# Kernel tuning notes

Hardware: AMD Instinct MI355X
Metric: run time of the kernel (lower is better)

## Reference

```python
import jax, jax.numpy as jnp
import numpy as np

N, E, Q = 50000, 500000, 100000
IN_DIM, HID, EDGE_DIM, NUM_CLASSES = 128, 128, 16, 2


def _glorot(key, shape):
    fan_in, fan_out = shape
    lim = (6.0 / (fan_in + fan_out)) ** 0.5
    return jax.random.uniform(key, shape, jnp.float32, -lim, lim)


def setup_inputs() -> dict:
    key = jax.random.key(0)
    ks = jax.random.split(key, 12)
    return {
        "node_feature": jax.random.normal(ks[0], (N, IN_DIM), jnp.float32),
        "edge_index": jax.random.randint(ks[1], (2, E), 0, N, jnp.int64),
        "edge_feature": jax.random.normal(ks[2], (E, EDGE_DIM), jnp.float32),
        "edge_label_index": jax.random.randint(ks[3], (2, Q), 0, N, jnp.int64),
        # conv1 params
        "c1_pre_W": _glorot(ks[4], (IN_DIM, IN_DIM)),
        "c1_pre_b": jnp.zeros((IN_DIM,), jnp.float32),
        "c1_msg_W": _glorot(ks[5], (2 * IN_DIM + EDGE_DIM, HID)),
        "c1_msg_b": jnp.zeros((HID,), jnp.float32),
        # conv2 params
        "c2_pre_W": _glorot(ks[6], (HID, HID)),
        "c2_pre_b": jnp.zeros((HID,), jnp.float32),
        "c2_msg_W": _glorot(ks[7], (2 * HID + EDGE_DIM, HID)),
        "c2_msg_b": jnp.zeros((HID,), jnp.float32),
        # link-prediction head
        "lp_W": _glorot(ks[8], (2 * HID, NUM_CLASSES)),
        "lp_b": jnp.zeros((NUM_CLASSES,), jnp.float32),
    }


def _mlp_message_conv(x, edge_index, edge_feature, pre_W, pre_b, msg_W, msg_b):
    # pre_conv: Linear + ReLU
    h = jax.nn.relu(x @ pre_W + pre_b)
    src, dst = edge_index[0], edge_index[1]
    # PyG default flow source_to_target: x_i = target, x_j = source
    x_i = h[dst]  # [E, d]
    x_j = h[src]  # [E, d]
    msg = jnp.concatenate([x_i, x_j, edge_feature], axis=1) @ msg_W + msg_b  # [E, out]
    # aggr='add' onto target nodes
    return jax.ops.segment_sum(msg, dst, num_segments=x.shape[0])


def reference(node_feature, edge_index, edge_feature, edge_label_index,
              c1_pre_W, c1_pre_b, c1_msg_W, c1_msg_b,
              c2_pre_W, c2_pre_b, c2_msg_W, c2_msg_b,
              lp_W, lp_b):
    # eval mode: dropout is identity
    x = jax.nn.relu(_mlp_message_conv(node_feature, edge_index, edge_feature,
                                      c1_pre_W, c1_pre_b, c1_msg_W, c1_msg_b))
    x = _mlp_message_conv(x, edge_index, edge_feature,
                          c2_pre_W, c2_pre_b, c2_msg_W, c2_msg_b)
    nodes_first = x[edge_label_index[0]]   # [Q, hid]
    nodes_second = x[edge_label_index[1]]  # [Q, hid]
    pred = jnp.concatenate([nodes_first, nodes_second], axis=-1) @ lp_W + lp_b
    return pred
```

## Files before the change

kernel.cpp:

```cpp
#include <hip/hip_runtime.h>
#include <cstdint>
#include <cstddef>


typedef __attribute__((ext_vector_type(8))) short short8;
typedef __attribute__((ext_vector_type(4))) float float4v;

__device__ __forceinline__ ushort f2b(float f) {
    uint u = __float_as_uint(f);
    u = u + 0x7fff + ((u >> 16) & 1);
    return (ushort)(u >> 16);
}
__device__ __forceinline__ float b2f(ushort h) {
    return __uint_as_float(((uint)h) << 16);
}
__device__ __forceinline__ uint pack2(float a, float b) {
    return (uint)f2b(a) | ((uint)f2b(b) << 16);
}

#define F_MSG     1
#define F_RELU    2
#define F_DEGBIAS 4
#define F_OUTB    8
#define F_IN32    16
#define F_HEAD    32

#define XS_STRIDE 72

__launch_bounds__(256, 2)
__global__ void gemm_mfma(const ushort* __restrict__ A, const ushort* __restrict__ B,
                          const ushort* __restrict__ EF, const float* __restrict__ A32,
                          const float* __restrict__ DEG, const ushort* __restrict__ Wt,
                          const float* __restrict__ bias, ushort* __restrict__ outB,
                          const float* __restrict__ lpW, float* __restrict__ z,
                          int M, int Kp, int flags)
{
    __shared__ ushort xs[128 * XS_STRIDE];
    __shared__ ushort ws[128 * XS_STRIDE];
    const int tid  = threadIdx.x;
    const int lane = tid & 63;
    const int wave = tid >> 6;
    const int row0 = blockIdx.x << 7;

    float4v acc[2][8];
#pragma unroll
    for (int m = 0; m < 2; ++m)
#pragma unroll
        for (int t = 0; t < 8; ++t) acc[m][t] = (float4v){0.f, 0.f, 0.f, 0.f};

    const int arow0 = (wave << 5) + (lane & 15);
    const int koff  = (lane >> 4) << 3;
    const int bcol  = lane & 15;

    for (int kt = 0; kt < Kp; kt += 64) {
        __syncthreads();
        for (int idx = tid; idx < 128 * 8; idx += 256) {
            const int n = idx >> 3;
            const int g = idx & 7;
            const uint4 v = *(const uint4*)&Wt[(size_t)n * Kp + kt + (g << 3)];
            *(uint4*)&ws[n * XS_STRIDE + (g << 3)] = v;
        }
        if (flags & F_MSG) {
            for (int idx = tid; idx < 128 * 8; idx += 256) {
                const int r  = idx >> 3;
                const int g  = idx & 7;
                const int gr = row0 + r;
                const int kk = kt + (g << 3);
                uint4 v = make_uint4(0, 0, 0, 0);
                if (gr < M) {
                    if (kk < 128) {
                        uint4 a = *(const uint4*)&A[((size_t)gr << 7) + kk];
                        const float d = DEG[gr];
                        uint* p = (uint*)&a;
#pragma unroll
                        for (int q = 0; q < 4; ++q)
                            p[q] = pack2(b2f((ushort)(p[q] & 0xffff)) * d,
                                         b2f((ushort)(p[q] >> 16)) * d);
                        v = a;
                    } else if (kk < 256) {
                        v = *(const uint4*)&B[((size_t)gr << 7) + kk - 128];
                    } else if (kk < 272) {
                        v = *(const uint4*)&EF[((size_t)gr << 4) + kk - 256];
                    }
                }
                *(uint4*)&xs[r * XS_STRIDE + (g << 3)] = v;
            }
        } else if (flags & F_IN32) {
            for (int idx = tid; idx < 128 * 8; idx += 256) {
                const int r  = idx >> 3;
                const int g  = idx & 7;
                const int gr = row0 + r;
                uint4 v = make_uint4(0, 0, 0, 0);
                if (gr < M) {
                    const float4 f0 = *(const float4*)&A32[((size_t)gr << 7) + kt + (g << 3)];
                    const float4 f1 = *(const float4*)&A32[((size_t)gr << 7) + kt + (g << 3) + 4];
                    v.x = pack2(f0.x, f0.y); v.y = pack2(f0.z, f0.w);
                    v.z = pack2(f1.x, f1.y); v.w = pack2(f1.z, f1.w);
                }
                *(uint4*)&xs[r * XS_STRIDE + (g << 3)] = v;
            }
        } else {
            for (int idx = tid; idx < 128 * 8; idx += 256) {
                const int r  = idx >> 3;
                const int g  = idx & 7;
                const int gr = row0 + r;
                uint4 v = make_uint4(0, 0, 0, 0);
                if (gr < M) v = *(const uint4*)&A[((size_t)gr << 7) + kt + (g << 3)];
                *(uint4*)&xs[r * XS_STRIDE + (g << 3)] = v;
            }
        }
        __syncthreads();
#pragma unroll
        for (int s = 0; s < 64; s += 32) {
            const short8 a0 = *(const short8*)&xs[arow0 * XS_STRIDE + s + koff];
            const short8 a1 = *(const short8*)&xs[(arow0 + 16) * XS_STRIDE + s + koff];
#pragma unroll
            for (int t = 0; t < 8; ++t) {
                const short8 bf = *(const short8*)&ws[((t << 4) + bcol) * XS_STRIDE + s + koff];
                acc[0][t] = __builtin_amdgcn_mfma_f32_16x16x32_bf16(a0, bf, acc[0][t], 0, 0, 0);
                acc[1][t] = __builtin_amdgcn_mfma_f32_16x16x32_bf16(a1, bf, acc[1][t], 0, 0, 0);
            }
        }
    }

    float bcv[8];
#pragma unroll
    for (int t = 0; t < 8; ++t) bcv[t] = bias[(t << 4) + bcol];

    if (flags & F_HEAD) {
        const float2* lw = (const float2*)lpW;
        float2 wa[8], wb[8];
#pragma unroll
        for (int t = 0; t < 8; ++t) {
            const int col = (t << 4) + bcol;
            wa[t] = lw[col];
            wb[t] = lw[128 + col];
        }
#pragma unroll
        for (int m = 0; m < 2; ++m) {
            const int rbase = row0 + (wave << 5) + (m << 4) + ((lane >> 4) << 2);
#pragma unroll
            for (int r = 0; r < 4; ++r) {
                const int row = rbase + r;
                const float d = (row < M) ? DEG[row] : 0.f;
                float za0 = 0.f, za1 = 0.f, zb0 = 0.f, zb1 = 0.f;
#pragma unroll
                for (int t = 0; t < 8; ++t) {
                    const float v = acc[m][t][r] + d * bcv[t];
                    za0 += v * wa[t].x; za1 += v * wa[t].y;
                    zb0 += v * wb[t].x; zb1 += v * wb[t].y;
                }
#pragma unroll
                for (int mk = 8; mk > 0; mk >>= 1) {
                    za0 += __shfl_xor(za0, mk);
                    za1 += __shfl_xor(za1, mk);
                    zb0 += __shfl_xor(zb0, mk);
                    zb1 += __shfl_xor(zb1, mk);
                }
                if (bcol == 0 && row < M)
                    *(float4*)&z[(size_t)row * 4] = make_float4(za0, za1, zb0, zb1);
            }
        }
    } else {
#pragma unroll
        for (int m = 0; m < 2; ++m) {
            const int rbase = row0 + (wave << 5) + (m << 4) + ((lane >> 4) << 2);
#pragma unroll
            for (int t = 0; t < 8; ++t) {
                const int col = (t << 4) + bcol;
#pragma unroll
                for (int r = 0; r < 4; ++r) {
                    const int row = rbase + r;
                    if (row >= M) continue;
                    float v = acc[m][t][r];
                    v += (flags & F_DEGBIAS) ? DEG[row] * bcv[t] : bcv[t];
                    if (flags & F_RELU) v = fmaxf(v, 0.f);
                    outB[((size_t)row << 7) + col] = f2b(v);
                }
            }
        }
    }
}

__launch_bounds__(256)
__global__ void prep(const float* __restrict__ c1pW, const float* __restrict__ c2pW,
                     const float* __restrict__ c1mW, const float* __restrict__ c2mW,
                     ushort* __restrict__ wtp1, ushort* __restrict__ wtp2,
                     ushort* __restrict__ wtm1, ushort* __restrict__ wtm2,
                     int* __restrict__ counts, int N)
{
    const int gtid = blockIdx.x * 256 + threadIdx.x;
    const int gstr = gridDim.x * 256;
    for (int i = gtid; i < N; i += gstr) counts[i] = 0;
    for (int idx = gtid; idx < 128 * 128; idx += gstr) {
        const int n = idx >> 7, k = idx & 127;
        wtp1[idx] = f2b(c1pW[(size_t)k * 128 + n]);
        wtp2[idx] = f2b(c2pW[(size_t)k * 128 + n]);
    }
    for (int idx = gtid; idx < 128 * 320; idx += gstr) {
        const int n = idx / 320, k = idx - n * 320;
        wtm1[idx] = (k < 272) ? f2b(c1mW[(size_t)k * 128 + n]) : (ushort)0;
        wtm2[idx] = (k < 272) ? f2b(c2mW[(size_t)k * 128 + n]) : (ushort)0;
    }
}

__launch_bounds__(256)
__global__ void hist_kernel(const int* __restrict__ ei, int* __restrict__ counts, int E)
{
    const int e = blockIdx.x * 256 + threadIdx.x;
    if (e < E) atomicAdd(&counts[ei[E + e]], 1);
}

__launch_bounds__(256)
__global__ void scan_phase1(const int* __restrict__ counts, int* __restrict__ rowstart,
                            int* __restrict__ blocksums, int N)
{
    __shared__ int sdata[256];
    const int t = threadIdx.x;
    const int i = blockIdx.x * 256 + t;
    const int v = (i < N) ? counts[i] : 0;
    sdata[t] = v;
    __syncthreads();
    for (int off = 1; off < 256; off <<= 1) {
        const int add = (t >= off) ? sdata[t - off] : 0;
        __syncthreads();
        sdata[t] += add;
        __syncthreads();
    }
    if (i < N) rowstart[i] = sdata[t] - v;
    if (t == 255) blocksums[blockIdx.x] = sdata[255];
}

__launch_bounds__(256)
__global__ void scan_phase23(const int* __restrict__ counts, const int* __restrict__ bs,
                             int* __restrict__ rowstart, int* __restrict__ cursor,
                             float* __restrict__ degf, int N, int E)
{
    __shared__ int sdata[256];
    const int t = threadIdx.x;
    const int vb = blockIdx.x;
    int part = 0;
    for (int j = t; j < vb; j += 256) part += bs[j];
    sdata[t] = part;
    __syncthreads();
    for (int s = 128; s > 0; s >>= 1) {
        if (t < s) sdata[t] += sdata[t + s];
        __syncthreads();
    }
    const int off = sdata[0];
    const int i = vb * 256 + t;
    if (i < N) {
        const int rs = rowstart[i] + off;
        rowstart[i] = rs;
        cursor[i]   = rs;
        degf[i]     = (float)counts[i];
    }
    if (vb == 0 && t == 0) rowstart[N] = E;
}

__launch_bounds__(256)
__global__ void build_elist(const int* __restrict__ ei, int* __restrict__ cursor,
                            int* __restrict__ esrc, int* __restrict__ eeid, int E)
{
    const int e = blockIdx.x * 256 + threadIdx.x;
    if (e >= E) return;
    const int d = ei[E + e];
    const int pos = atomicAdd(&cursor[d], 1);
    esrc[pos] = ei[e];
    eeid[pos] = e;
}

__launch_bounds__(256)
__global__ void gather(const int* __restrict__ esrc, const int* __restrict__ eeid,
                       const int* __restrict__ rowstart,
                       const ushort* __restrict__ h, ushort* __restrict__ agg,
                       const float* __restrict__ ef, ushort* __restrict__ aggef,
                       int N, int doEf)
{
    const int tid = threadIdx.x;
    if (doEf) {
        const int nvb = (N + 15) / 16;
        const int lane16 = tid & 15;
        for (int vb = blockIdx.x; vb < nvb; vb += gridDim.x) {
            const int node = vb * 16 + (tid >> 4);
            if (node >= N) continue;
            const int beg = rowstart[node];
            const int end = rowstart[node + 1];
            float acc = 0.f;
            for (int k = beg; k < end; ++k)
                acc += ef[((size_t)eeid[k] << 4) + lane16];
            aggef[((size_t)node << 4) + lane16] = f2b(acc);
        }
    }
    {
        const int nvb = (N + 3) / 4;
        const int lane = tid & 63;
        const int wave = tid >> 6;
        for (int vb = blockIdx.x; vb < nvb; vb += gridDim.x) {
            const int node = vb * 4 + wave;
            if (node >= N) continue;
            const int beg = rowstart[node];
            const int end = rowstart[node + 1];
            float ax = 0.f, ay = 0.f;
            int k = beg;
            for (; k + 3 < end; k += 4) {
                const int s0 = esrc[k];
                const int s1 = esrc[k + 1];
                const int s2 = esrc[k + 2];
                const int s3 = esrc[k + 3];
                const uint v0 = *(const uint*)&h[((size_t)s0 << 7) + (lane << 1)];
                const uint v1 = *(const uint*)&h[((size_t)s1 << 7) + (lane << 1)];
                const uint v2 = *(const uint*)&h[((size_t)s2 << 7) + (lane << 1)];
                const uint v3 = *(const uint*)&h[((size_t)s3 << 7) + (lane << 1)];
                ax += b2f((ushort)(v0 & 0xffff)) + b2f((ushort)(v1 & 0xffff))
                    + b2f((ushort)(v2 & 0xffff)) + b2f((ushort)(v3 & 0xffff));
                ay += b2f((ushort)(v0 >> 16)) + b2f((ushort)(v1 >> 16))
                    + b2f((ushort)(v2 >> 16)) + b2f((ushort)(v3 >> 16));
            }
            for (; k < end; ++k) {
                const uint v = *(const uint*)&h[((size_t)esrc[k] << 7) + (lane << 1)];
                ax += b2f((ushort)(v & 0xffff));
                ay += b2f((ushort)(v >> 16));
            }
            *(uint*)&agg[((size_t)node << 7) + (lane << 1)] = pack2(ax, ay);
        }
    }
}

__launch_bounds__(256)
__global__ void head_kernel(const float4* __restrict__ z, const int* __restrict__ eli,
                            const float* __restrict__ lpb, float* __restrict__ out, int Q)
{
    const int q = blockIdx.x * 256 + threadIdx.x;
    if (q >= Q) return;
    const int a = eli[q];
    const int b = eli[Q + q];
    const float4 za = z[a];
    const float4 zb = z[b];
    float2 o = make_float2(za.x + zb.z + lpb[0], za.y + zb.w + lpb[1]);
    *(float2*)&out[(size_t)q * 2] = o;
}

extern "C" void kernel_launch(void* const* d_in, const int* in_sizes, int n_in,
                              void* d_out, int out_size, void* d_ws, size_t ws_size,
                              hipStream_t stream)
{
    const float* nf   = (const float*)d_in[0];
    const int*   ei   = (const int*)d_in[1];
    const float* ef   = (const float*)d_in[2];
    const int*   eli  = (const int*)d_in[3];
    const float* c1pW = (const float*)d_in[4];
    const float* c1pb = (const float*)d_in[5];
    const float* c1mW = (const float*)d_in[6];
    const float* c1mb = (const float*)d_in[7];
    const float* c2pW = (const float*)d_in[8];
    const float* c2pb = (const float*)d_in[9];
    const float* c2mW = (const float*)d_in[10];
    const float* c2mb = (const float*)d_in[11];
    const float* lpW  = (const float*)d_in[12];
    const float* lpb  = (const float*)d_in[13];
    float* out = (float*)d_out;

    const int N = in_sizes[0] / 128;
    const int E = in_sizes[1] / 2;
    const int Q = in_sizes[3] / 2;

    float* DEG = (float*)d_ws;
    float* z   = DEG + N;
    int* counts    = (int*)(z + (size_t)N * 4);
    int* rowstart  = counts + N;
    int* cursor    = rowstart + N + 1;
    int* blocksums = cursor + N;
    int* esrc      = blocksums + 1024;
    int* eeid      = esrc + E;
    uintptr_t up = (uintptr_t)(eeid + E);
    up = (up + 15) & ~(uintptr_t)15;
    ushort* h_bf   = (ushort*)up;
    ushort* agg_bf = h_bf   + (size_t)N * 128;
    ushort* x1_bf  = agg_bf + (size_t)N * 128;
    ushort* ef_bf  = x1_bf  + (size_t)N * 128;
    ushort* wtp1   = ef_bf  + (size_t)N * 16;
    ushort* wtm1   = wtp1 + 128 * 128;
    ushort* wtp2   = wtm1 + 128 * 320;
    ushort* wtm2   = wtp2 + 128 * 128;

    const int gemmGrid = (N + 127) / 128;
    const int eGrid    = (E + 255) / 256;
    const int nGrid    = (N + 255) / 256;
    const int gGrid    = (N + 3) / 4;
    const int headGrid = (Q + 255) / 256;

    prep<<<nGrid, 256, 0, stream>>>(c1pW, c2pW, c1mW, c2mW, wtp1, wtp2, wtm1, wtm2,
                                    counts, N);
    hist_kernel<<<eGrid, 256, 0, stream>>>(ei, counts, E);
    scan_phase1<<<nGrid, 256, 0, stream>>>(counts, rowstart, blocksums, N);
    scan_phase23<<<nGrid, 256, 0, stream>>>(counts, blocksums, rowstart, cursor, DEG, N, E);
    build_elist<<<eGrid, 256, 0, stream>>>(ei, cursor, esrc, eeid, E);

    gemm_mfma<<<gemmGrid, 256, 0, stream>>>(nullptr, nullptr, nullptr, nf, DEG, wtp1,
                                            c1pb, h_bf, nullptr, nullptr, N, 128,
                                            F_RELU | F_OUTB | F_IN32);
    gather<<<gGrid, 256, 0, stream>>>(esrc, eeid, rowstart, h_bf, agg_bf, ef, ef_bf, N, 1);
    gemm_mfma<<<gemmGrid, 256, 0, stream>>>(h_bf, agg_bf, ef_bf, nullptr, DEG, wtm1,
                                            c1mb, x1_bf, nullptr, nullptr, N, 320,
                                            F_MSG | F_RELU | F_DEGBIAS | F_OUTB);

    gemm_mfma<<<gemmGrid, 256, 0, stream>>>(x1_bf, nullptr, nullptr, nullptr, DEG, wtp2,
                                            c2pb, h_bf, nullptr, nullptr, N, 128,
                                            F_RELU | F_OUTB);
    gather<<<gGrid, 256, 0, stream>>>(esrc, eeid, rowstart, h_bf, agg_bf, nullptr, nullptr, N, 0);
    gemm_mfma<<<gemmGrid, 256, 0, stream>>>(h_bf, agg_bf, ef_bf, nullptr, DEG, wtm2,
                                            c2mb, nullptr, lpW, z, N, 320,
                                            F_MSG | F_DEGBIAS | F_HEAD);

    head_kernel<<<headGrid, 256, 0, stream>>>((const float4*)z, eli, lpb, out, Q);
}
```

Measured before the change: 331.8 us.

## Split node features into column halves and pin each half to an XCD group

The pre-conv GEMMs now write h in a planar layout of two 64-column halves. The gather kernel maps blocks so that XCDs 0-3 only read the first half and XCDs 4-7 only the second, using 32 lanes per node. The message GEMM's A load is adjusted to read the split layout. The goal is to shrink each XCD's random-gather working set so more of it stays in its L2, at the cost of relying on round-robin block-to-XCD dispatch and issuing narrower 128-byte row reads.

```diff
diff --git a/kernel.cpp b/kernel.cpp
--- a/kernel.cpp
+++ b/kernel.cpp
@@ -24,6 +24,7 @@
 #define F_OUTB    8
 #define F_IN32    16
 #define F_HEAD    32
+#define F_OUTH    64
 
 #define XS_STRIDE 72
 
@@ -51,6 +52,7 @@
     const int arow0 = (wave << 5) + (lane & 15);
     const int koff  = (lane >> 4) << 3;
     const int bcol  = lane & 15;
+    const size_t halfSz = (size_t)M * 64;
 
     for (int kt = 0; kt < Kp; kt += 64) {
         __syncthreads();
@@ -69,7 +71,9 @@
                 uint4 v = make_uint4(0, 0, 0, 0);
                 if (gr < M) {
                     if (kk < 128) {
-                        uint4 a = *(const uint4*)&A[((size_t)gr << 7) + kk];
+                        const int hh = kk >> 6;
+                        uint4 a = *(const uint4*)&A[(size_t)hh * halfSz
+                                                    + ((size_t)gr << 6) + (kk & 63)];
                         const float d = DEG[gr];
                         uint* p = (uint*)&a;
 #pragma unroll
@@ -168,6 +172,10 @@
 #pragma unroll
             for (int t = 0; t < 8; ++t) {
                 const int col = (t << 4) + bcol;
+                const size_t obase = (flags & F_OUTH)
+                    ? (size_t)(col >> 6) * halfSz + (col & 63)
+                    : (size_t)col;
+                const int oshift = (flags & F_OUTH) ? 6 : 7;
 #pragma unroll
                 for (int r = 0; r < 4; ++r) {
                     const int row = rbase + r;
@@ -175,7 +183,7 @@
                     float v = acc[m][t][r];
                     v += (flags & F_DEGBIAS) ? DEG[row] * bcv[t] : bcv[t];
                     if (flags & F_RELU) v = fmaxf(v, 0.f);
-                    outB[((size_t)row << 7) + col] = f2b(v);
+                    outB[obase + ((size_t)row << oshift)] = f2b(v);
                 }
             }
         }
@@ -293,37 +301,38 @@
         }
     }
     {
-        const int nvb = (N + 3) / 4;
-        const int lane = tid & 63;
-        const int wave = tid >> 6;
-        for (int vb = blockIdx.x; vb < nvb; vb += gridDim.x) {
-            const int node = vb * 4 + wave;
-            if (node >= N) continue;
-            const int beg = rowstart[node];
-            const int end = rowstart[node + 1];
-            float ax = 0.f, ay = 0.f;
-            int k = beg;
-            for (; k + 3 < end; k += 4) {
-                const int s0 = esrc[k];
-                const int s1 = esrc[k + 1];
-                const int s2 = esrc[k + 2];
-                const int s3 = esrc[k + 3];
-                const uint v0 = *(const uint*)&h[((size_t)s0 << 7) + (lane << 1)];
-                const uint v1 = *(const uint*)&h[((size_t)s1 << 7) + (lane << 1)];
-                const uint v2 = *(const uint*)&h[((size_t)s2 << 7) + (lane << 1)];
-                const uint v3 = *(const uint*)&h[((size_t)s3 << 7) + (lane << 1)];
-                ax += b2f((ushort)(v0 & 0xffff)) + b2f((ushort)(v1 & 0xffff))
-                    + b2f((ushort)(v2 & 0xffff)) + b2f((ushort)(v3 & 0xffff));
-                ay += b2f((ushort)(v0 >> 16)) + b2f((ushort)(v1 >> 16))
-                    + b2f((ushort)(v2 >> 16)) + b2f((ushort)(v3 >> 16));
-            }
-            for (; k < end; ++k) {
-                const uint v = *(const uint*)&h[((size_t)esrc[k] << 7) + (lane << 1)];
-                ax += b2f((ushort)(v & 0xffff));
-                ay += b2f((ushort)(v >> 16));
-            }
-            *(uint*)&agg[((size_t)node << 7) + (lane << 1)] = pack2(ax, ay);
-        }
+        const int b    = blockIdx.x;
+        const int xcd  = b & 7;
+        const int half = xcd >> 2;
+        const int chunk = (b >> 3) * 4 + (xcd & 3);
+        const int node = chunk * 8 + (tid >> 5);
+        if (node >= N) return;
+        const int l = tid & 31;
+        const ushort* hh = h + (size_t)half * ((size_t)N << 6);
+        const int beg = rowstart[node];
+        const int end = rowstart[node + 1];
+        float ax = 0.f, ay = 0.f;
+        int k = beg;
+        for (; k + 3 < end; k += 4) {
+            const int s0 = esrc[k];
+            const int s1 = esrc[k + 1];
+            const int s2 = esrc[k + 2];
+            const int s3 = esrc[k + 3];
+            const uint v0 = *(const uint*)&hh[((size_t)s0 << 6) + (l << 1)];
+            const uint v1 = *(const uint*)&hh[((size_t)s1 << 6) + (l << 1)];
+            const uint v2 = *(const uint*)&hh[((size_t)s2 << 6) + (l << 1)];
+            const uint v3 = *(const uint*)&hh[((size_t)s3 << 6) + (l << 1)];
+            ax += b2f((ushort)(v0 & 0xffff)) + b2f((ushort)(v1 & 0xffff))
+                + b2f((ushort)(v2 & 0xffff)) + b2f((ushort)(v3 & 0xffff));
+            ay += b2f((ushort)(v0 >> 16)) + b2f((ushort)(v1 >> 16))
+                + b2f((ushort)(v2 >> 16)) + b2f((ushort)(v3 >> 16));
+        }
+        for (; k < end; ++k) {
+            const uint v = *(const uint*)&hh[((size_t)esrc[k] << 6) + (l << 1)];
+            ax += b2f((ushort)(v & 0xffff));
+            ay += b2f((ushort)(v >> 16));
+        }
+        *(uint*)&agg[((size_t)node << 7) + (half << 6) + (l << 1)] = pack2(ax, ay);
     }
 }
 
@@ -387,8 +396,9 @@
     const int gemmGrid = (N + 127) / 128;
     const int eGrid    = (E + 255) / 256;
     const int nGrid    = (N + 255) / 256;
-    const int gGrid    = (N + 3) / 4;
     const int headGrid = (Q + 255) / 256;
+    const int nchunks  = (N + 7) / 8;
+    const int gGrid    = ((nchunks + 3) / 4) * 8;
 
     prep<<<nGrid, 256, 0, stream>>>(c1pW, c2pW, c1mW, c2mW, wtp1, wtp2, wtm1, wtm2,
                                     counts, N);
@@ -399,7 +409,7 @@
 
     gemm_mfma<<<gemmGrid, 256, 0, stream>>>(nullptr, nullptr, nullptr, nf, DEG, wtp1,
                                             c1pb, h_bf, nullptr, nullptr, N, 128,
-                                            F_RELU | F_OUTB | F_IN32);
+                                            F_RELU | F_OUTH | F_IN32);
     gather<<<gGrid, 256, 0, stream>>>(esrc, eeid, rowstart, h_bf, agg_bf, ef, ef_bf, N, 1);
     gemm_mfma<<<gemmGrid, 256, 0, stream>>>(h_bf, agg_bf, ef_bf, nullptr, DEG, wtm1,
                                             c1mb, x1_bf, nullptr, nullptr, N, 320,
@@ -407,7 +417,7 @@
 
     gemm_mfma<<<gemmGrid, 256, 0, stream>>>(x1_bf, nullptr, nullptr, nullptr, DEG, wtp2,
                                             c2pb, h_bf, nullptr, nullptr, N, 128,
-                                            F_RELU | F_OUTB);
+                                            F_RELU | F_OUTH);
     gather<<<gGrid, 256, 0, stream>>>(esrc, eeid, rowstart, h_bf, agg_bf, nullptr, nullptr, N, 0);
     gemm_mfma<<<gemmGrid, 256, 0, stream>>>(h_bf, agg_bf, ef_bf, nullptr, DEG, wtm2,
                                             c2mb, nullptr, lpW, z, N, 320,
```

New measurement: 343.0 us. 3.4% more time.

## Double-buffer GEMM tiles via register prefetch and pack edge list as int2

Applied to the files above, without the earlier changes.

The MFMA GEMM now prefetches the next K-chunk of weights and activations into registers while computing the current chunk from a second LDS buffer, with one barrier per iteration. The goal is to overlap global load latency with MFMA work. The separate source and edge-id arrays are merged into one int2 edge list. This saves a second index load when edge features are aggregated, but the index stream doubles in size in the gather that uses only sources. It also doubles LDS use and raises register pressure.

```diff
diff --git a/kernel.cpp b/kernel.cpp
--- a/kernel.cpp
+++ b/kernel.cpp
@@ -35,12 +35,13 @@
                           const float* __restrict__ lpW, float* __restrict__ z,
                           int M, int Kp, int flags)
 {
-    __shared__ ushort xs[128 * XS_STRIDE];
-    __shared__ ushort ws[128 * XS_STRIDE];
+    __shared__ ushort xs[2][128 * XS_STRIDE];
+    __shared__ ushort ws[2][128 * XS_STRIDE];
     const int tid  = threadIdx.x;
     const int lane = tid & 63;
     const int wave = tid >> 6;
     const int row0 = blockIdx.x << 7;
+    const int nch  = Kp >> 6;
 
     float4v acc[2][8];
 #pragma unroll
@@ -52,75 +53,145 @@
     const int koff  = (lane >> 4) << 3;
     const int bcol  = lane & 15;
 
-    for (int kt = 0; kt < Kp; kt += 64) {
-        __syncthreads();
-        for (int idx = tid; idx < 128 * 8; idx += 256) {
-            const int n = idx >> 3;
-            const int g = idx & 7;
-            const uint4 v = *(const uint4*)&Wt[(size_t)n * Kp + kt + (g << 3)];
-            *(uint4*)&ws[n * XS_STRIDE + (g << 3)] = v;
-        }
+    uint4  wreg[4];
+    uint4  xreg[4];
+    float4 fa[4], fb[4];
+    float  dsc[4];
+
+    auto loadW = [&](int kt) {
+#pragma unroll
+        for (int j = 0; j < 4; ++j) {
+            const int idx = tid + j * 256;
+            const int n = idx >> 3, g = idx & 7;
+            wreg[j] = *(const uint4*)&Wt[(size_t)n * Kp + kt + (g << 3)];
+        }
+    };
+    auto storeW = [&](int b) {
+#pragma unroll
+        for (int j = 0; j < 4; ++j) {
+            const int idx = tid + j * 256;
+            const int n = idx >> 3, g = idx & 7;
+            *(uint4*)&ws[b][n * XS_STRIDE + (g << 3)] = wreg[j];
+        }
+    };
+    auto loadX = [&](int kt) {
         if (flags & F_MSG) {
-            for (int idx = tid; idx < 128 * 8; idx += 256) {
-                const int r  = idx >> 3;
-                const int g  = idx & 7;
+            if (kt < 128) {
+#pragma unroll
+                for (int j = 0; j < 4; ++j) {
+                    const int idx = tid + j * 256;
+                    const int r = idx >> 3, g = idx & 7;
+                    const int gr = row0 + r;
+                    if (gr < M) {
+                        xreg[j] = *(const uint4*)&A[((size_t)gr << 7) + kt + (g << 3)];
+                        dsc[j]  = DEG[gr];
+                    } else { xreg[j] = make_uint4(0,0,0,0); dsc[j] = 0.f; }
+                }
+            } else if (kt < 256) {
+#pragma unroll
+                for (int j = 0; j < 4; ++j) {
+                    const int idx = tid + j * 256;
+                    const int r = idx >> 3, g = idx & 7;
+                    const int gr = row0 + r;
+                    xreg[j] = (gr < M)
+                        ? *(const uint4*)&B[((size_t)gr << 7) + (kt - 128) + (g << 3)]
+                        : make_uint4(0,0,0,0);
+                }
+            } else {
+#pragma unroll
+                for (int j = 0; j < 4; ++j) {
+                    const int idx = tid + j * 256;
+                    const int r = idx >> 3, g = idx & 7;
+                    const int gr = row0 + r;
+                    xreg[j] = (g < 2 && gr < M)
+                        ? *(const uint4*)&EF[((size_t)gr << 4) + (g << 3)]
+                        : make_uint4(0,0,0,0);
+                }
+            }
+        } else if (flags & F_IN32) {
+#pragma unroll
+            for (int j = 0; j < 4; ++j) {
+                const int idx = tid + j * 256;
+                const int r = idx >> 3, g = idx & 7;
                 const int gr = row0 + r;
-                const int kk = kt + (g << 3);
-                uint4 v = make_uint4(0, 0, 0, 0);
                 if (gr < M) {
-                    if (kk < 128) {
-                        uint4 a = *(const uint4*)&A[((size_t)gr << 7) + kk];
-                        const float d = DEG[gr];
-                        uint* p = (uint*)&a;
-#pragma unroll
-                        for (int q = 0; q < 4; ++q)
-                            p[q] = pack2(b2f((ushort)(p[q] & 0xffff)) * d,
-                                         b2f((ushort)(p[q] >> 16)) * d);
-                        v = a;
-                    } else if (kk < 256) {
-                        v = *(const uint4*)&B[((size_t)gr << 7) + kk - 128];
-                    } else if (kk < 272) {
-                        v = *(const uint4*)&EF[((size_t)gr << 4) + kk - 256];
-                    }
-                }
-                *(uint4*)&xs[r * XS_STRIDE + (g << 3)] = v;
+                    fa[j] = *(const float4*)&A32[((size_t)gr << 7) + kt + (g << 3)];
+                    fb[j] = *(const float4*)&A32[((size_t)gr << 7) + kt + (g << 3) + 4];
+                } else {
+                    fa[j] = make_float4(0,0,0,0);
+                    fb[j] = make_float4(0,0,0,0);
+                }
+            }
+        } else {
+#pragma unroll
+            for (int j = 0; j < 4; ++j) {
+                const int idx = tid + j * 256;
+                const int r = idx >> 3, g = idx & 7;
+                const int gr = row0 + r;
+                xreg[j] = (gr < M)
+                    ? *(const uint4*)&A[((size_t)gr << 7) + kt + (g << 3)]
+                    : make_uint4(0,0,0,0);
+            }
+        }
+    };
+    auto storeX = [&](int b, int kt) {
+        if ((flags & F_MSG) && kt < 128) {
+#pragma unroll
+            for (int j = 0; j < 4; ++j) {
+                const int idx = tid + j * 256;
+                const int r = idx >> 3, g = idx & 7;
+                uint4 a = xreg[j];
+                const float d = dsc[j];
+                uint* p = (uint*)&a;
+#pragma unroll
+                for (int q = 0; q < 4; ++q)
+                    p[q] = pack2(b2f((ushort)(p[q] & 0xffff)) * d,
+                                 b2f((ushort)(p[q] >> 16)) * d);
+                *(uint4*)&xs[b][r * XS_STRIDE + (g << 3)] = a;
             }
         } else if (flags & F_IN32) {
-            for (int idx = tid; idx < 128 * 8; idx += 256) {
-                const int r  = idx >> 3;
-                const int g  = idx & 7;
-                const int gr = row0 + r;
-                uint4 v = make_uint4(0, 0, 0, 0);
-                if (gr < M) {
-                    const float4 f0 = *(const float4*)&A32[((size_t)gr << 7) + kt + (g << 3)];
-                    const float4 f1 = *(const float4*)&A32[((size_t)gr << 7) + kt + (g << 3) + 4];
-                    v.x = pack2(f0.x, f0.y); v.y = pack2(f0.z, f0.w);
-                    v.z = pack2(f1.x, f1.y); v.w = pack2(f1.z, f1.w);
-                }
-                *(uint4*)&xs[r * XS_STRIDE + (g << 3)] = v;
+#pragma unroll
+            for (int j = 0; j < 4; ++j) {
+                const int idx = tid + j * 256;
+                const int r = idx >> 3, g = idx & 7;
+                uint4 v;
+                v.x = pack2(fa[j].x, fa[j].y); v.y = pack2(fa[j].z, fa[j].w);
+                v.z = pack2(fb[j].x, fb[j].y); v.w = pack2(fb[j].z, fb[j].w);
+                *(uint4*)&xs[b][r * XS_STRIDE + (g << 3)] = v;
             }
         } else {
-            for (int idx = tid; idx < 128 * 8; idx += 256) {
-                const int r  = idx >> 3;
-                const int g  = idx & 7;
-                const int gr = row0 + r;
-                uint4 v = make_uint4(0, 0, 0, 0);
-                if (gr < M) v = *(const uint4*)&A[((size_t)gr << 7) + kt + (g << 3)];
-                *(uint4*)&xs[r * XS_STRIDE + (g << 3)] = v;
-            }
-        }
-        __syncthreads();
+#pragma unroll
+            for (int j = 0; j < 4; ++j) {
+                const int idx = tid + j * 256;
+                const int r = idx >> 3, g = idx & 7;
+                *(uint4*)&xs[b][r * XS_STRIDE + (g << 3)] = xreg[j];
+            }
+        }
+    };
+
+    loadW(0);
+    loadX(0);
+    storeW(0);
+    storeX(0, 0);
+    __syncthreads();
+
+    for (int c = 0; c < nch; ++c) {
+        const int cur = c & 1;
+        const int ktn = (c + 1) << 6;
+        if (c + 1 < nch) { loadW(ktn); loadX(ktn); }
 #pragma unroll
         for (int s = 0; s < 64; s += 32) {
-            const short8 a0 = *(const short8*)&xs[arow0 * XS_STRIDE + s + koff];
-            const short8 a1 = *(const short8*)&xs[(arow0 + 16) * XS_STRIDE + s + koff];
+            const short8 a0 = *(const short8*)&xs[cur][arow0 * XS_STRIDE + s + koff];
+            const short8 a1 = *(const short8*)&xs[cur][(arow0 + 16) * XS_STRIDE + s + koff];
 #pragma unroll
             for (int t = 0; t < 8; ++t) {
-                const short8 bf = *(const short8*)&ws[((t << 4) + bcol) * XS_STRIDE + s + koff];
+                const short8 bf = *(const short8*)&ws[cur][((t << 4) + bcol) * XS_STRIDE + s + koff];
                 acc[0][t] = __builtin_amdgcn_mfma_f32_16x16x32_bf16(a0, bf, acc[0][t], 0, 0, 0);
                 acc[1][t] = __builtin_amdgcn_mfma_f32_16x16x32_bf16(a1, bf, acc[1][t], 0, 0, 0);
             }
         }
+        if (c + 1 < nch) { storeW(cur ^ 1); storeX(cur ^ 1, ktn); }
+        __syncthreads();
     }
 
     float bcv[8];
@@ -260,19 +331,17 @@
 
 __launch_bounds__(256)
 __global__ void build_elist(const int* __restrict__ ei, int* __restrict__ cursor,
-                            int* __restrict__ esrc, int* __restrict__ eeid, int E)
+                            int2* __restrict__ elist, int E)
 {
     const int e = blockIdx.x * 256 + threadIdx.x;
     if (e >= E) return;
     const int d = ei[E + e];
     const int pos = atomicAdd(&cursor[d], 1);
-    esrc[pos] = ei[e];
-    eeid[pos] = e;
-}
-
-__launch_bounds__(256)
-__global__ void gather(const int* __restrict__ esrc, const int* __restrict__ eeid,
-                       const int* __restrict__ rowstart,
+    elist[pos] = make_int2(ei[e], e);
+}
+
+__launch_bounds__(256)
+__global__ void gather(const int2* __restrict__ elist, const int* __restrict__ rowstart,
                        const ushort* __restrict__ h, ushort* __restrict__ agg,
                        const float* __restrict__ ef, ushort* __restrict__ aggef,
                        int N, int doEf)
@@ -288,7 +357,7 @@
             const int end = rowstart[node + 1];
             float acc = 0.f;
             for (int k = beg; k < end; ++k)
-                acc += ef[((size_t)eeid[k] << 4) + lane16];
+                acc += ef[((size_t)elist[k].y << 4) + lane16];
             aggef[((size_t)node << 4) + lane16] = f2b(acc);
         }
     }
@@ -304,10 +373,10 @@
             float ax = 0.f, ay = 0.f;
             int k = beg;
             for (; k + 3 < end; k += 4) {
-                const int s0 = esrc[k];
-                const int s1 = esrc[k + 1];
-                const int s2 = esrc[k + 2];
-                const int s3 = esrc[k + 3];
+                const int s0 = elist[k].x;
+                const int s1 = elist[k + 1].x;
+                const int s2 = elist[k + 2].x;
+                const int s3 = elist[k + 3].x;
                 const uint v0 = *(const uint*)&h[((size_t)s0 << 7) + (lane << 1)];
                 const uint v1 = *(const uint*)&h[((size_t)s1 << 7) + (lane << 1)];
                 const uint v2 = *(const uint*)&h[((size_t)s2 << 7) + (lane << 1)];
@@ -318,7 +387,7 @@
                     + b2f((ushort)(v2 >> 16)) + b2f((ushort)(v3 >> 16));
             }
             for (; k < end; ++k) {
-                const uint v = *(const uint*)&h[((size_t)esrc[k] << 7) + (lane << 1)];
+                const uint v = *(const uint*)&h[((size_t)elist[k].x << 7) + (lane << 1)];
                 ax += b2f((ushort)(v & 0xffff));
                 ay += b2f((ushort)(v >> 16));
             }
@@ -371,9 +440,10 @@
     int* rowstart  = counts + N;
     int* cursor    = rowstart + N + 1;
     int* blocksums = cursor + N;
-    int* esrc      = blocksums + 1024;
-    int* eeid      = esrc + E;
-    uintptr_t up = (uintptr_t)(eeid + E);
+    uintptr_t ep8 = (uintptr_t)(blocksums + 1024);
+    ep8 = (ep8 + 7) & ~(uintptr_t)7;
+    int2* elist = (int2*)ep8;
+    uintptr_t up = (uintptr_t)(elist + E);
     up = (up + 15) & ~(uintptr_t)15;
     ushort* h_bf   = (ushort*)up;
     ushort* agg_bf = h_bf   + (size_t)N * 128;
@@ -395,12 +465,12 @@
     hist_kernel<<<eGrid, 256, 0, stream>>>(ei, counts, E);
     scan_phase1<<<nGrid, 256, 0, stream>>>(counts, rowstart, blocksums, N);
     scan_phase23<<<nGrid, 256, 0, stream>>>(counts, blocksums, rowstart, cursor, DEG, N, E);
-    build_elist<<<eGrid, 256, 0, stream>>>(ei, cursor, esrc, eeid, E);
+    build_elist<<<eGrid, 256, 0, stream>>>(ei, cursor, elist, E);
 
     gemm_mfma<<<gemmGrid, 256, 0, stream>>>(nullptr, nullptr, nullptr, nf, DEG, wtp1,
                                             c1pb, h_bf, nullptr, nullptr, N, 128,
                                             F_RELU | F_OUTB | F_IN32);
-    gather<<<gGrid, 256, 0, stream>>>(esrc, eeid, rowstart, h_bf, agg_bf, ef, ef_bf, N, 1);
+    gather<<<gGrid, 256, 0, stream>>>(elist, rowstart, h_bf, agg_bf, ef, ef_bf, N, 1);
     gemm_mfma<<<gemmGrid, 256, 0, stream>>>(h_bf, agg_bf, ef_bf, nullptr, DEG, wtm1,
                                             c1mb, x1_bf, nullptr, nullptr, N, 320,
                                             F_MSG | F_RELU | F_DEGBIAS | F_OUTB);
@@ -408,7 +478,7 @@
     gemm_mfma<<<gemmGrid, 256, 0, stream>>>(x1_bf, nullptr, nullptr, nullptr, DEG, wtp2,
                                             c2pb, h_bf, nullptr, nullptr, N, 128,
                                             F_RELU | F_OUTB);
-    gather<<<gGrid, 256, 0, stream>>>(esrc, eeid, rowstart, h_bf, agg_bf, nullptr, nullptr, N, 0);
+    gather<<<gGrid, 256, 0, stream>>>(elist, rowstart, h_bf, agg_bf, nullptr, nullptr, N, 0);
     gemm_mfma<<<gemmGrid, 256, 0, stream>>>(h_bf, agg_bf, ef_bf, nullptr, DEG, wtm2,
                                             c2mb, nullptr, lpW, z, N, 320,
                                             F_MSG | F_DEGBIAS | F_HEAD);
```

After: 344.1 us. 1.04x slower.
